# Performance work log

Measured on AMD Instinct MI355X. Metric: run time of the kernel, lower is better.

The kernel has to match this reference:

```python
import jax, jax.numpy as jnp
import numpy as np

B, N_NODES, D, H, L, DFF, K = 16, 512, 256, 8, 4, 1024, 128
DH = D // H


def setup_inputs() -> dict:
    key = jax.random.key(0)
    ks = jax.random.split(key, 16)
    x = jax.random.normal(ks[0], (B, N_NODES, D), jnp.float32)
    d = jax.random.uniform(ks[1], (B, N_NODES, N_NODES), jnp.float32)
    dist = 0.5 * (d + jnp.swapaxes(d, -1, -2))
    dist = dist * (1.0 - jnp.eye(N_NODES, dtype=jnp.float32))  # zero diagonal
    mask = jnp.ones((B, 1, N_NODES), dtype=bool)
    s = 0.02
    Wq = jax.random.normal(ks[2], (L, D, D), jnp.float32) * s
    Wk = jax.random.normal(ks[3], (L, D, D), jnp.float32) * s
    Wv = jax.random.normal(ks[4], (L, D, D), jnp.float32) * s
    Wo = jax.random.normal(ks[5], (L, D, D), jnp.float32) * s
    W1 = jax.random.normal(ks[6], (L, D, DFF), jnp.float32) * s
    W2 = jax.random.normal(ks[7], (L, DFF, D), jnp.float32) * s
    ln1_g = jnp.ones((L, D), jnp.float32)
    ln1_b = jnp.zeros((L, D), jnp.float32)
    ln2_g = jnp.ones((L, D), jnp.float32)
    ln2_b = jnp.zeros((L, D), jnp.float32)
    gamma = jnp.ones((D,), jnp.float32)
    beta = jnp.zeros((D,), jnp.float32)
    return dict(x=x, dist=dist, mask=mask, Wq=Wq, Wk=Wk, Wv=Wv, Wo=Wo, W1=W1, W2=W2,
                ln1_g=ln1_g, ln1_b=ln1_b, ln2_g=ln2_g, ln2_b=ln2_b, gamma=gamma, beta=beta)


def _ln(x, g, b, eps=1e-6):
    mu = jnp.mean(x, axis=-1, keepdims=True)
    var = jnp.mean((x - mu) ** 2, axis=-1, keepdims=True)
    return (x - mu) * jax.lax.rsqrt(var + eps) * g + b


def _afps(scores, dist, k):
    # scores: [H, n, n] attention probs; dist: [n, n]; mask assumed all-True.
    s = jnp.sum(jnp.mean(scores, axis=0), axis=-2)            # [n] column sums
    d = dist / jnp.max(dist) + (s / jnp.max(s))[:, None] * 0.1  # [n, n]
    n = d.shape[0]
    mind0 = d[:, 0]                                            # min dist to {0}
    sel0 = jnp.zeros((n,), bool).at[0].set(True)

    def body(carry, _):
        mind, sel = carry
        cand = jnp.where(sel, -jnp.inf, mind)  # exclude already-selected
        new = jnp.argmax(cand)
        return (jnp.minimum(mind, d[:, new]), sel.at[new].set(True)), new

    _, picks = jax.lax.scan(body, (mind0, sel0), None, length=k - 1)
    return jnp.concatenate([jnp.zeros((1,), picks.dtype), picks])  # [k]


def reference(x, dist, mask, Wq, Wk, Wv, Wo, W1, W2, ln1_g, ln1_b, ln2_g, ln2_b, gamma, beta):
    key_mask = mask[:, :, None, :]  # [B,1,1,n] broadcast over heads/queries
    inv_sqrt = np.float32(1.0 / np.sqrt(DH))
    scores = None
    for i in range(L):
        h = _ln(x, ln1_g[i], ln1_b[i])
        q = (h @ Wq[i]).reshape(B, N_NODES, H, DH).transpose(0, 2, 1, 3)
        kk = (h @ Wk[i]).reshape(B, N_NODES, H, DH).transpose(0, 2, 1, 3)
        v = (h @ Wv[i]).reshape(B, N_NODES, H, DH).transpose(0, 2, 1, 3)
        logits = jnp.einsum('bhqd,bhkd->bhqk', q, kk) * inv_sqrt - dist[:, None]
        logits = jnp.where(key_mask, logits, jnp.float32(-1e9))
        scores = jax.nn.softmax(logits, axis=-1)               # [B,H,n,n]
        attn = jnp.einsum('bhqk,bhkd->bhqd', scores, v)
        x = x + attn.transpose(0, 2, 1, 3).reshape(B, N_NODES, D) @ Wo[i]
        h2 = _ln(x, ln2_g[i], ln2_b[i])
        x = x + jax.nn.gelu(h2 @ W1[i]) @ W2[i]
    # AFPS index selection runs under no_grad in the original
    idx = jax.vmap(lambda sc, dd: _afps(sc, dd, K))(
        jax.lax.stop_gradient(scores), jax.lax.stop_gradient(dist))  # [B,K]
    pooled = jnp.mean(jnp.take_along_axis(x, idx[:, :, None], axis=1), axis=1)  # [B,D]
    return _ln(pooled, gamma, beta)
```

## Files before the change

kernel.cpp:

```cpp
#include <hip/hip_runtime.h>
#include <hip/hip_bf16.h>
#include <math.h>

#define BB 16
#define NN 512
#define DD 256
#define HH 8
#define LL 4
#define DFF 1024
#define KSEL 128
#define DH 32

typedef __attribute__((ext_vector_type(8))) short bf16x8v;
typedef __attribute__((ext_vector_type(4))) float f32x4v;

static const size_t X_B    = 0;
static const size_t QKVB_B = 8388608;
static const size_t VT_B   = 20971520;
static const size_t FFN_B  = 8388608;
static const size_t H_B    = 25165824;
static const size_t ATT_B  = 29360128;
static const size_t WQKV_B = 33554432;
static const size_t WO_B   = 35127296;
static const size_t W1T_B  = 35651584;
static const size_t W2T_B  = 37748736;
static const size_t S_B    = 39845888;
static const size_t MAXD_B = 39878656;
static const size_t IDX_B  = 39878720;

__device__ __forceinline__ float gelu_f(float x) {
  float x3 = x * x * x;
  return 0.5f * x * (1.f + tanhf(0.7978845608028654f * (x + 0.044715f * x3)));
}

__device__ __forceinline__ short bf16raw(float v) {
  __hip_bfloat16 h = __float2bfloat16(v);
  return *reinterpret_cast<short*>(&h);
}

__device__ __forceinline__ float blk_sum_256(float v, float* stmp) {
  #pragma unroll
  for (int o = 32; o > 0; o >>= 1) v += __shfl_down(v, o, 64);
  if ((threadIdx.x & 63) == 0) stmp[threadIdx.x >> 6] = v;
  __syncthreads();
  if (threadIdx.x == 0) stmp[0] = stmp[0] + stmp[1] + stmp[2] + stmp[3];
  __syncthreads();
  float r = stmp[0];
  __syncthreads();
  return r;
}

__global__ void copy_kernel(const float4* __restrict__ src, float4* __restrict__ dst, int n) {
  int i = blockIdx.x * blockDim.x + threadIdx.x;
  if (i < n) dst[i] = src[i];
}

__global__ __launch_bounds__(256) void cast_weights_kernel(
    const float* __restrict__ Wq, const float* __restrict__ Wk,
    const float* __restrict__ Wv, const float* __restrict__ Wo,
    const float* __restrict__ W1, const float* __restrict__ W2,
    __hip_bfloat16* __restrict__ qkvT, __hip_bfloat16* __restrict__ WoT,
    __hip_bfloat16* __restrict__ W1T, __hip_bfloat16* __restrict__ W2T) {
  int i = blockIdx.x * 256 + threadIdx.x;
  if (i < 786432) {
    int l = i / 196608, r = i % 196608;
    int n = r >> 8, k = r & 255;
    const float* src = (n < 256) ? Wq : (n < 512 ? Wk : Wv);
    qkvT[i] = __float2bfloat16(src[l * 65536 + k * 256 + (n & 255)]);
  } else if (i < 1048576) {
    int j = i - 786432;
    int l = j >> 16, r = j & 65535;
    int n = r >> 8, k = r & 255;
    WoT[j] = __float2bfloat16(Wo[l * 65536 + k * 256 + n]);
  } else if (i < 2097152) {
    int j = i - 1048576;
    int l = j >> 18, r = j & 262143;
    int n = r >> 8, k = r & 255;
    W1T[j] = __float2bfloat16(W1[l * 262144 + k * 1024 + n]);
  } else {
    int j = i - 2097152;
    int l = j >> 18, r = j & 262143;
    int n = r >> 10, k = r & 1023;
    W2T[j] = __float2bfloat16(W2[l * 262144 + k * 256 + n]);
  }
}

__global__ __launch_bounds__(256) void ln_cast_kernel(const float* __restrict__ in,
                                                      const float* __restrict__ g,
                                                      const float* __restrict__ bb,
                                                      __hip_bfloat16* __restrict__ out) {
  __shared__ float stmp[4];
  size_t row = blockIdx.x;
  int d = threadIdx.x;
  float v = in[row * DD + d];
  float mu = blk_sum_256(v, stmp) * (1.0f / DD);
  float diff = v - mu;
  float var = blk_sum_256(diff * diff, stmp) * (1.0f / DD);
  out[row * DD + d] = __float2bfloat16(diff * rsqrtf(var + 1e-6f) * g[d] + bb[d]);
}

template <int MODE>
__global__ __launch_bounds__(256) void mfma_gemm(const __hip_bfloat16* __restrict__ A,
                                                 const __hip_bfloat16* __restrict__ Bt,
                                                 const float* __restrict__ Res,
                                                 void* __restrict__ Cv,
                                                 __hip_bfloat16* __restrict__ Vto,
                                                 int M, int N, int Kd) {
  __shared__ short As[64 * 40];
  __shared__ short Bs[64 * 40];
  const int tid = threadIdx.x;
  const int w = tid >> 6, lane = tid & 63;
  const int m16 = lane & 15, quad = lane >> 4;
  const int bm = blockIdx.y << 6, bn = blockIdx.x << 6;
  const int srow = tid >> 2, scol = (tid & 3) << 3;

  f32x4v zero = {0.f, 0.f, 0.f, 0.f};
  f32x4v acc[4];
  #pragma unroll
  for (int nt = 0; nt < 4; ++nt) acc[nt] = zero;

  const short* Ag = (const short*)A;
  const short* Bg = (const short*)Bt;

  for (int k0 = 0; k0 < Kd; k0 += 32) {
    *(bf16x8v*)&As[srow * 40 + scol] =
        *(const bf16x8v*)(Ag + (size_t)(bm + srow) * Kd + k0 + scol);
    *(bf16x8v*)&Bs[srow * 40 + scol] =
        *(const bf16x8v*)(Bg + (size_t)(bn + srow) * Kd + k0 + scol);
    __syncthreads();
    bf16x8v af = *(bf16x8v*)&As[(w * 16 + m16) * 40 + (quad << 3)];
    #pragma unroll
    for (int nt = 0; nt < 4; ++nt) {
      bf16x8v bf = *(bf16x8v*)&Bs[(nt * 16 + m16) * 40 + (quad << 3)];
      acc[nt] = __builtin_amdgcn_mfma_f32_16x16x32_bf16(af, bf, acc[nt], 0, 0, 0);
    }
    __syncthreads();
  }

  const int erow = bm + w * 16 + quad * 4;
  #pragma unroll
  for (int nt = 0; nt < 4; ++nt) {
    int col = bn + nt * 16 + m16;
    if (MODE == 3) {
      if (col < 512) {
        #pragma unroll
        for (int r = 0; r < 4; ++r)
          ((__hip_bfloat16*)Cv)[(size_t)(erow + r) * 768 + col] =
              __float2bfloat16(acc[nt][r]);
      } else {
        short4 pk;
        pk.x = bf16raw(acc[nt][0]); pk.y = bf16raw(acc[nt][1]);
        pk.z = bf16raw(acc[nt][2]); pk.w = bf16raw(acc[nt][3]);
        int bb2 = erow >> 9, key = erow & 511, dim = col - 512;
        *(short4*)((short*)Vto + (size_t)bb2 * 131072 + (size_t)dim * 512 + key) = pk;
      }
    } else {
      #pragma unroll
      for (int r = 0; r < 4; ++r) {
        float v = acc[nt][r];
        size_t off = (size_t)(erow + r) * N + col;
        if (MODE == 1) ((float*)Cv)[off] = v + Res[off];
        else ((__hip_bfloat16*)Cv)[off] = __float2bfloat16(gelu_f(v));
      }
    }
  }
}

__global__ __launch_bounds__(512) void attn_kernel(const __hip_bfloat16* __restrict__ qkvb,
                                                   const __hip_bfloat16* __restrict__ vt,
                                                   const float* __restrict__ dist,
                                                   __hip_bfloat16* __restrict__ outg,
                                                   float* __restrict__ s_acc,
                                                   int accum) {
  __shared__ float Pf[8][16 * 36];
  const int tid = threadIdx.x;
  const int h = tid >> 6, lane = tid & 63;
  const int m16 = lane & 15, quad = lane >> 4;
  const int b = blockIdx.y;
  const int qbase = blockIdx.x * 16;
  const float scale = 0.17677669529663687f;
  const f32x4v zero = {0.f, 0.f, 0.f, 0.f};

  const short* qkvs = (const short*)qkvb;
  const short* vts = (const short*)vt + (size_t)b * 131072;
  float* Pw = Pf[h];

  bf16x8v qf = *(const bf16x8v*)(qkvs + ((size_t)(b * NN + qbase + m16)) * 768 + h * 32 + (quad << 3));

  int drow[4];
  #pragma unroll
  for (int r = 0; r < 4; ++r) drow[r] = (b * NN + qbase + quad * 4 + r) * NN;

  f32x4v accO0 = zero, accO1 = zero;
  float laccL[4] = {0.f, 0.f, 0.f, 0.f};

  for (int t0 = 0; t0 < NN; t0 += 32) {
    bf16x8v kf0 = *(const bf16x8v*)(qkvs + ((size_t)(b * NN + t0 + m16)) * 768 + 256 + h * 32 + (quad << 3));
    bf16x8v kf1 = *(const bf16x8v*)(qkvs + ((size_t)(b * NN + t0 + 16 + m16)) * 768 + 256 + h * 32 + (quad << 3));
    f32x4v s0 = __builtin_amdgcn_mfma_f32_16x16x32_bf16(qf, kf0, zero, 0, 0, 0);
    f32x4v s1 = __builtin_amdgcn_mfma_f32_16x16x32_bf16(qf, kf1, zero, 0, 0, 0);
    #pragma unroll
    for (int r = 0; r < 4; ++r) {
      float e0 = __expf(fmaf(s0[r], scale, -dist[drow[r] + t0 + m16]));
      float e1 = __expf(fmaf(s1[r], scale, -dist[drow[r] + t0 + 16 + m16]));
      laccL[r] += e0 + e1;
      Pw[(quad * 4 + r) * 36 + m16] = e0;
      Pw[(quad * 4 + r) * 36 + 16 + m16] = e1;
    }
    bf16x8v pfr;
    {
      const float* pr = &Pw[m16 * 36 + (quad << 3)];
      float4 pa = *(const float4*)pr;
      float4 pb = *(const float4*)(pr + 4);
      pfr[0] = bf16raw(pa.x); pfr[1] = bf16raw(pa.y);
      pfr[2] = bf16raw(pa.z); pfr[3] = bf16raw(pa.w);
      pfr[4] = bf16raw(pb.x); pfr[5] = bf16raw(pb.y);
      pfr[6] = bf16raw(pb.z); pfr[7] = bf16raw(pb.w);
    }
    bf16x8v vf0 = *(const bf16x8v*)(vts + (size_t)(h * 32 + m16) * 512 + t0 + (quad << 3));
    bf16x8v vf1 = *(const bf16x8v*)(vts + (size_t)(h * 32 + 16 + m16) * 512 + t0 + (quad << 3));
    accO0 = __builtin_amdgcn_mfma_f32_16x16x32_bf16(pfr, vf0, accO0, 0, 0, 0);
    accO1 = __builtin_amdgcn_mfma_f32_16x16x32_bf16(pfr, vf1, accO1, 0, 0, 0);
  }

  float invl[4];
  #pragma unroll
  for (int r = 0; r < 4; ++r) {
    float t = laccL[r];
    t += __shfl_xor(t, 1, 64); t += __shfl_xor(t, 2, 64);
    t += __shfl_xor(t, 4, 64); t += __shfl_xor(t, 8, 64);
    invl[r] = 1.f / t;
  }

  #pragma unroll
  for (int r = 0; r < 4; ++r) {
    size_t orow = (size_t)(b * NN + qbase + quad * 4 + r) * DD + h * 32;
    outg[orow + m16] = __float2bfloat16(accO0[r] * invl[r]);
    outg[orow + 16 + m16] = __float2bfloat16(accO1[r] * invl[r]);
  }

  if (accum) {
    for (int t0 = 0; t0 < NN; t0 += 32) {
      bf16x8v kf0 = *(const bf16x8v*)(qkvs + ((size_t)(b * NN + t0 + m16)) * 768 + 256 + h * 32 + (quad << 3));
      bf16x8v kf1 = *(const bf16x8v*)(qkvs + ((size_t)(b * NN + t0 + 16 + m16)) * 768 + 256 + h * 32 + (quad << 3));
      f32x4v s0 = __builtin_amdgcn_mfma_f32_16x16x32_bf16(qf, kf0, zero, 0, 0, 0);
      f32x4v s1 = __builtin_amdgcn_mfma_f32_16x16x32_bf16(qf, kf1, zero, 0, 0, 0);
      float p0 = 0.f, p1 = 0.f;
      #pragma unroll
      for (int r = 0; r < 4; ++r) {
        p0 += __expf(fmaf(s0[r], scale, -dist[drow[r] + t0 + m16])) * invl[r];
        p1 += __expf(fmaf(s1[r], scale, -dist[drow[r] + t0 + 16 + m16])) * invl[r];
      }
      p0 += __shfl_xor(p0, 16, 64); p0 += __shfl_xor(p0, 32, 64);
      p1 += __shfl_xor(p1, 16, 64); p1 += __shfl_xor(p1, 32, 64);
      if (quad == 0) {
        atomicAdd(&s_acc[b * NN + t0 + m16], p0 * 0.125f);
        atomicAdd(&s_acc[b * NN + t0 + 16 + m16], p1 * 0.125f);
      }
    }
  }
}

__global__ __launch_bounds__(256) void maxd_kernel(const float* __restrict__ dist,
                                                   unsigned int* __restrict__ maxd) {
  const int b = blockIdx.y;
  const int tid = threadIdx.x;
  const float4* p = (const float4*)(dist + (size_t)b * NN * NN) +
                    blockIdx.x * 8192 + tid;
  float m = 0.f;
  #pragma unroll 8
  for (int i = 0; i < 32; ++i) {
    float4 v = p[i * 256];
    m = fmaxf(m, fmaxf(fmaxf(v.x, v.y), fmaxf(v.z, v.w)));
  }
  #pragma unroll
  for (int o = 32; o > 0; o >>= 1) m = fmaxf(m, __shfl_xor(m, o, 64));
  __shared__ float wm[4];
  if ((tid & 63) == 0) wm[tid >> 6] = m;
  __syncthreads();
  if (tid == 0) {
    float mm = fmaxf(fmaxf(wm[0], wm[1]), fmaxf(wm[2], wm[3]));
    atomicMax(&maxd[b], __float_as_uint(mm));
  }
}

__global__ __launch_bounds__(64) void afps_select_kernel(const float* __restrict__ dist,
                                                         const float* __restrict__ s,
                                                         const unsigned int* __restrict__ maxd,
                                                         int* __restrict__ idx_out) {
  const int b = blockIdx.x;
  const int lane = threadIdx.x;
  const float* db = dist + (size_t)b * NN * NN;

  float sv[8];
  float ms = 0.f;
  #pragma unroll
  for (int r = 0; r < 8; ++r) {
    sv[r] = s[b * NN + r * 64 + lane];
    ms = fmaxf(ms, sv[r]);
  }
  #pragma unroll
  for (int o = 32; o > 0; o >>= 1) ms = fmaxf(ms, __shfl_xor(ms, o, 64));

  const float invmaxd = 1.0f / __uint_as_float(maxd[b]);
  float sn[8], mind[8];
  #pragma unroll
  for (int r = 0; r < 8; ++r) {
    sn[r] = (sv[r] / ms) * 0.1f;
    mind[r] = db[r * 64 + lane] * invmaxd + sn[r];
  }
  unsigned selm = (lane == 0) ? 1u : 0u;
  if (lane == 0) idx_out[b * KSEL + 0] = 0;

  int specIdx = -1;
  float sreg[8];

  for (int it = 1; it < KSEL; ++it) {
    unsigned long long b1 = 0ull, b2 = 0ull;
    #pragma unroll
    for (int r = 0; r < 8; ++r) {
      unsigned long long pk =
          ((selm >> r) & 1u) ? 0ull
            : (((unsigned long long)__float_as_uint(mind[r])) << 32) |
              (unsigned)(511 - (r * 64 + lane));
      if (pk > b1) { b2 = b1; b1 = pk; }
      else if (pk > b2) b2 = pk;
    }
    #pragma unroll
    for (int o = 32; o > 0; o >>= 1) {
      unsigned long long o1 = __shfl_xor(b1, o, 64);
      unsigned long long o2 = __shfl_xor(b2, o, 64);
      unsigned long long n1 = b1 > o1 ? b1 : o1;
      unsigned long long lo = b1 > o1 ? o1 : b1;
      unsigned long long n2 = b2 > o2 ? b2 : o2;
      b2 = lo > n2 ? lo : n2;
      b1 = n1;
    }
    const int nw = 511 - (int)(unsigned)(b1 & 0xffffffffu);
    const int sec = 511 - (int)(unsigned)(b2 & 0xffffffffu);

    float rowv[8];
    if (nw == specIdx) {
      #pragma unroll
      for (int r = 0; r < 8; ++r) rowv[r] = sreg[r];
    } else {
      const float* row = db + (size_t)nw * NN;
      #pragma unroll
      for (int r = 0; r < 8; ++r) rowv[r] = row[r * 64 + lane];
    }
    {
      const float* srow = db + (size_t)sec * NN;
      #pragma unroll
      for (int r = 0; r < 8; ++r) sreg[r] = srow[r * 64 + lane];
      specIdx = sec;
    }
    if (lane == (nw & 63)) selm |= 1u << (nw >> 6);
    if (lane == 0) idx_out[b * KSEL + it] = nw;
    #pragma unroll
    for (int r = 0; r < 8; ++r)
      mind[r] = fminf(mind[r], fmaf(rowv[r], invmaxd, sn[r]));
  }
}

__global__ __launch_bounds__(256) void pool_ln_kernel(const float* __restrict__ x,
                                                      const int* __restrict__ idx,
                                                      const float* __restrict__ gamma,
                                                      const float* __restrict__ beta,
                                                      float* __restrict__ out) {
  __shared__ float stmp[4];
  __shared__ int sIdx[KSEL];
  const int b = blockIdx.x;
  const int d = threadIdx.x;
  if (d < KSEL) sIdx[d] = idx[b * KSEL + d];
  __syncthreads();
  float acc = 0.f;
  #pragma unroll 4
  for (int kk = 0; kk < KSEL; ++kk)
    acc += x[((size_t)b * NN + sIdx[kk]) * DD + d];
  float p = acc * (1.0f / KSEL);
  float mu = blk_sum_256(p, stmp) * (1.0f / DD);
  float diff = p - mu;
  float var = blk_sum_256(diff * diff, stmp) * (1.0f / DD);
  out[b * DD + d] = diff * rsqrtf(var + 1e-6f) * gamma[d] + beta[d];
}

extern "C" void kernel_launch(void* const* d_in, const int* in_sizes, int n_in,
                              void* d_out, int out_size, void* d_ws, size_t ws_size,
                              hipStream_t stream) {
  (void)in_sizes; (void)n_in; (void)out_size; (void)ws_size;
  const float* x_in  = (const float*)d_in[0];
  const float* dist  = (const float*)d_in[1];
  const float* Wq    = (const float*)d_in[3];
  const float* Wk    = (const float*)d_in[4];
  const float* Wv    = (const float*)d_in[5];
  const float* Wo    = (const float*)d_in[6];
  const float* W1    = (const float*)d_in[7];
  const float* W2    = (const float*)d_in[8];
  const float* ln1_g = (const float*)d_in[9];
  const float* ln1_b = (const float*)d_in[10];
  const float* ln2_g = (const float*)d_in[11];
  const float* ln2_b = (const float*)d_in[12];
  const float* gamma = (const float*)d_in[13];
  const float* beta  = (const float*)d_in[14];

  char* wsb = (char*)d_ws;
  float* x              = (float*)(wsb + X_B);
  __hip_bfloat16* qkvb  = (__hip_bfloat16*)(wsb + QKVB_B);
  __hip_bfloat16* vtb   = (__hip_bfloat16*)(wsb + VT_B);
  __hip_bfloat16* ffn   = (__hip_bfloat16*)(wsb + FFN_B);
  __hip_bfloat16* hb    = (__hip_bfloat16*)(wsb + H_B);
  __hip_bfloat16* ab    = (__hip_bfloat16*)(wsb + ATT_B);
  __hip_bfloat16* WqkvT = (__hip_bfloat16*)(wsb + WQKV_B);
  __hip_bfloat16* WoT   = (__hip_bfloat16*)(wsb + WO_B);
  __hip_bfloat16* W1T   = (__hip_bfloat16*)(wsb + W1T_B);
  __hip_bfloat16* W2T   = (__hip_bfloat16*)(wsb + W2T_B);
  float* sbuf = (float*)(wsb + S_B);
  unsigned int* maxdb = (unsigned int*)(wsb + MAXD_B);
  int*   idxb = (int*)(wsb + IDX_B);
  float* out  = (float*)d_out;

  copy_kernel<<<2048, 256, 0, stream>>>((const float4*)x_in, (float4*)x, 524288);
  hipMemsetAsync(sbuf, 0, BB * NN * sizeof(float) + 64, stream);
  cast_weights_kernel<<<12288, 256, 0, stream>>>(Wq, Wk, Wv, Wo, W1, W2,
                                                 WqkvT, WoT, W1T, W2T);
  maxd_kernel<<<dim3(8, BB), 256, 0, stream>>>(dist, maxdb);

  const int M = BB * NN;
  dim3 gqkv(768 / 64, M / 64);
  dim3 go(DD / 64, M / 64);
  dim3 gf(DFF / 64, M / 64);
  dim3 ga(NN / 16, BB);

  for (int l = 0; l < LL; ++l) {
    ln_cast_kernel<<<M, 256, 0, stream>>>(x, ln1_g + l * DD, ln1_b + l * DD, hb);
    mfma_gemm<3><<<gqkv, 256, 0, stream>>>(hb, WqkvT + (size_t)l * 768 * 256, nullptr,
                                           qkvb, vtb, M, 768, 256);
    attn_kernel<<<ga, 512, 0, stream>>>(qkvb, vtb, dist, ab, sbuf, (l == LL - 1) ? 1 : 0);
    if (l == LL - 1) {
      afps_select_kernel<<<BB, 64, 0, stream>>>(dist, sbuf, maxdb, idxb);
    }
    mfma_gemm<1><<<go, 256, 0, stream>>>(ab, WoT + (size_t)l * 65536, x, x, nullptr, M, DD, 256);
    ln_cast_kernel<<<M, 256, 0, stream>>>(x, ln2_g + l * DD, ln2_b + l * DD, hb);
    mfma_gemm<2><<<gf, 256, 0, stream>>>(hb, W1T + (size_t)l * 262144, nullptr,
                                         ffn, nullptr, M, DFF, 256);
    mfma_gemm<1><<<go, 256, 0, stream>>>(ffn, W2T + (size_t)l * 262144, x, x, nullptr, M, DD, 1024);
  }
  pool_ln_kernel<<<BB, 256, 0, stream>>>(x, idxb, gamma, beta, out);
}
```

Baseline: 700.5 us.

## Fuse LayerNorm into QKV/FFN1 GEMMs, drop input copy, deepen AFPS speculation

LayerNorm is now computed inside the GEMM prologue: each block normalizes its 64 rows of fp32 x into a full-K bf16 LDS tile, which removes the separate ln_cast kernel and the bf16 h buffer round trip. The initial copy of x_in into the workspace is removed by reading x_in directly in layer 0 and using it as the residual source. The AFPS selection loop now keeps two speculatively prefetched distance rows instead of one. The cost is that LN work is repeated across every N-tile block (12 or 16 times per row) and the A tile in LDS grows to about 33KB, which may reduce occupancy.

```diff
diff --git a/kernel.cpp b/kernel.cpp
--- a/kernel.cpp
+++ b/kernel.cpp
@@ -18,7 +18,6 @@
 static const size_t QKVB_B = 8388608;
 static const size_t VT_B   = 20971520;
 static const size_t FFN_B  = 8388608;
-static const size_t H_B    = 25165824;
 static const size_t ATT_B  = 29360128;
 static const size_t WQKV_B = 33554432;
 static const size_t WO_B   = 35127296;
@@ -50,10 +49,6 @@
   return r;
 }
 
-__global__ void copy_kernel(const float4* __restrict__ src, float4* __restrict__ dst, int n) {
-  int i = blockIdx.x * blockDim.x + threadIdx.x;
-  if (i < n) dst[i] = src[i];
-}
 
 __global__ __launch_bounds__(256) void cast_weights_kernel(
     const float* __restrict__ Wq, const float* __restrict__ Wk,
@@ -85,50 +80,68 @@
   }
 }
 
-__global__ __launch_bounds__(256) void ln_cast_kernel(const float* __restrict__ in,
-                                                      const float* __restrict__ g,
-                                                      const float* __restrict__ bb,
-                                                      __hip_bfloat16* __restrict__ out) {
-  __shared__ float stmp[4];
-  size_t row = blockIdx.x;
-  int d = threadIdx.x;
-  float v = in[row * DD + d];
-  float mu = blk_sum_256(v, stmp) * (1.0f / DD);
-  float diff = v - mu;
-  float var = blk_sum_256(diff * diff, stmp) * (1.0f / DD);
-  out[row * DD + d] = __float2bfloat16(diff * rsqrtf(var + 1e-6f) * g[d] + bb[d]);
-}
-
 template <int MODE>
-__global__ __launch_bounds__(256) void mfma_gemm(const __hip_bfloat16* __restrict__ A,
-                                                 const __hip_bfloat16* __restrict__ Bt,
-                                                 const float* __restrict__ Res,
-                                                 void* __restrict__ Cv,
-                                                 __hip_bfloat16* __restrict__ Vto,
-                                                 int M, int N, int Kd) {
-  __shared__ short As[64 * 40];
+__global__ __launch_bounds__(256) void ln_gemm(const float* __restrict__ Xf,
+                                               const float* __restrict__ g,
+                                               const float* __restrict__ bb,
+                                               const __hip_bfloat16* __restrict__ Bt,
+                                               void* __restrict__ Cv,
+                                               __hip_bfloat16* __restrict__ Vto,
+                                               int N) {
+  __shared__ short As[64 * 264];
   __shared__ short Bs[64 * 40];
   const int tid = threadIdx.x;
   const int w = tid >> 6, lane = tid & 63;
   const int m16 = lane & 15, quad = lane >> 4;
   const int bm = blockIdx.y << 6, bn = blockIdx.x << 6;
+
+  {
+    const int row = tid >> 2, seg = (tid & 3) << 6;
+    const float* xr = Xf + (size_t)(bm + row) * 256 + seg;
+    float s1 = 0.f;
+    #pragma unroll
+    for (int i = 0; i < 16; ++i) {
+      float4 v = ((const float4*)xr)[i];
+      s1 += v.x + v.y + v.z + v.w;
+    }
+    s1 += __shfl_xor(s1, 1, 64); s1 += __shfl_xor(s1, 2, 64);
+    const float mu = s1 * (1.f / 256.f);
+    float s2 = 0.f;
+    #pragma unroll
+    for (int i = 0; i < 16; ++i) {
+      float4 v = ((const float4*)xr)[i];
+      float a0 = v.x - mu, a1 = v.y - mu, a2 = v.z - mu, a3 = v.w - mu;
+      s2 += a0 * a0 + a1 * a1 + a2 * a2 + a3 * a3;
+    }
+    s2 += __shfl_xor(s2, 1, 64); s2 += __shfl_xor(s2, 2, 64);
+    const float rsig = rsqrtf(s2 * (1.f / 256.f) + 1e-6f);
+    short* dst = &As[row * 264 + seg];
+    #pragma unroll
+    for (int i = 0; i < 16; ++i) {
+      float4 v = ((const float4*)xr)[i];
+      float4 gg = ((const float4*)(g + seg))[i];
+      float4 bv = ((const float4*)(bb + seg))[i];
+      short4 o;
+      o.x = bf16raw((v.x - mu) * rsig * gg.x + bv.x);
+      o.y = bf16raw((v.y - mu) * rsig * gg.y + bv.y);
+      o.z = bf16raw((v.z - mu) * rsig * gg.z + bv.z);
+      o.w = bf16raw((v.w - mu) * rsig * gg.w + bv.w);
+      *(short4*)(dst + i * 4) = o;
+    }
+  }
+  __syncthreads();
+
+  f32x4v acc[4];
+  #pragma unroll
+  for (int nt = 0; nt < 4; ++nt) acc[nt] = (f32x4v){0.f, 0.f, 0.f, 0.f};
+  const short* Bg = (const short*)Bt;
   const int srow = tid >> 2, scol = (tid & 3) << 3;
 
-  f32x4v zero = {0.f, 0.f, 0.f, 0.f};
-  f32x4v acc[4];
-  #pragma unroll
-  for (int nt = 0; nt < 4; ++nt) acc[nt] = zero;
-
-  const short* Ag = (const short*)A;
-  const short* Bg = (const short*)Bt;
-
-  for (int k0 = 0; k0 < Kd; k0 += 32) {
-    *(bf16x8v*)&As[srow * 40 + scol] =
-        *(const bf16x8v*)(Ag + (size_t)(bm + srow) * Kd + k0 + scol);
+  for (int k0 = 0; k0 < 256; k0 += 32) {
     *(bf16x8v*)&Bs[srow * 40 + scol] =
-        *(const bf16x8v*)(Bg + (size_t)(bn + srow) * Kd + k0 + scol);
+        *(const bf16x8v*)(Bg + (size_t)(bn + srow) * 256 + k0 + scol);
     __syncthreads();
-    bf16x8v af = *(bf16x8v*)&As[(w * 16 + m16) * 40 + (quad << 3)];
+    bf16x8v af = *(bf16x8v*)&As[(w * 16 + m16) * 264 + k0 + (quad << 3)];
     #pragma unroll
     for (int nt = 0; nt < 4; ++nt) {
       bf16x8v bf = *(bf16x8v*)&Bs[(nt * 16 + m16) * 40 + (quad << 3)];
@@ -156,12 +169,56 @@
       }
     } else {
       #pragma unroll
-      for (int r = 0; r < 4; ++r) {
-        float v = acc[nt][r];
-        size_t off = (size_t)(erow + r) * N + col;
-        if (MODE == 1) ((float*)Cv)[off] = v + Res[off];
-        else ((__hip_bfloat16*)Cv)[off] = __float2bfloat16(gelu_f(v));
-      }
+      for (int r = 0; r < 4; ++r)
+        ((__hip_bfloat16*)Cv)[(size_t)(erow + r) * N + col] =
+            __float2bfloat16(gelu_f(acc[nt][r]));
+    }
+  }
+}
+
+__global__ __launch_bounds__(256) void mfma_gemm_res(const __hip_bfloat16* __restrict__ A,
+                                                     const __hip_bfloat16* __restrict__ Bt,
+                                                     const float* __restrict__ Res,
+                                                     float* __restrict__ C,
+                                                     int M, int N, int Kd) {
+  __shared__ short As[64 * 40];
+  __shared__ short Bs[64 * 40];
+  const int tid = threadIdx.x;
+  const int w = tid >> 6, lane = tid & 63;
+  const int m16 = lane & 15, quad = lane >> 4;
+  const int bm = blockIdx.y << 6, bn = blockIdx.x << 6;
+  const int srow = tid >> 2, scol = (tid & 3) << 3;
+
+  f32x4v acc[4];
+  #pragma unroll
+  for (int nt = 0; nt < 4; ++nt) acc[nt] = (f32x4v){0.f, 0.f, 0.f, 0.f};
+
+  const short* Ag = (const short*)A;
+  const short* Bg = (const short*)Bt;
+
+  for (int k0 = 0; k0 < Kd; k0 += 32) {
+    *(bf16x8v*)&As[srow * 40 + scol] =
+        *(const bf16x8v*)(Ag + (size_t)(bm + srow) * Kd + k0 + scol);
+    *(bf16x8v*)&Bs[srow * 40 + scol] =
+        *(const bf16x8v*)(Bg + (size_t)(bn + srow) * Kd + k0 + scol);
+    __syncthreads();
+    bf16x8v af = *(bf16x8v*)&As[(w * 16 + m16) * 40 + (quad << 3)];
+    #pragma unroll
+    for (int nt = 0; nt < 4; ++nt) {
+      bf16x8v bf = *(bf16x8v*)&Bs[(nt * 16 + m16) * 40 + (quad << 3)];
+      acc[nt] = __builtin_amdgcn_mfma_f32_16x16x32_bf16(af, bf, acc[nt], 0, 0, 0);
+    }
+    __syncthreads();
+  }
+
+  const int erow = bm + w * 16 + quad * 4;
+  #pragma unroll
+  for (int nt = 0; nt < 4; ++nt) {
+    int col = bn + nt * 16 + m16;
+    #pragma unroll
+    for (int r = 0; r < 4; ++r) {
+      size_t off = (size_t)(erow + r) * N + col;
+      C[off] = acc[nt][r] + Res[off];
     }
   }
 }
@@ -312,8 +369,8 @@
   unsigned selm = (lane == 0) ? 1u : 0u;
   if (lane == 0) idx_out[b * KSEL + 0] = 0;
 
-  int specIdx = -1;
-  float sreg[8];
+  int spec0 = -1, spec1 = -1;
+  float sreg0[8], sreg1[8];
 
   for (int it = 1; it < KSEL; ++it) {
     unsigned long long b1 = 0ull, b2 = 0ull;
@@ -340,19 +397,25 @@
     const int sec = 511 - (int)(unsigned)(b2 & 0xffffffffu);
 
     float rowv[8];
-    if (nw == specIdx) {
-      #pragma unroll
-      for (int r = 0; r < 8; ++r) rowv[r] = sreg[r];
+    if (nw == spec0) {
+      #pragma unroll
+      for (int r = 0; r < 8; ++r) rowv[r] = sreg0[r];
+    } else if (nw == spec1) {
+      #pragma unroll
+      for (int r = 0; r < 8; ++r) rowv[r] = sreg1[r];
     } else {
       const float* row = db + (size_t)nw * NN;
       #pragma unroll
       for (int r = 0; r < 8; ++r) rowv[r] = row[r * 64 + lane];
     }
     {
+      #pragma unroll
+      for (int r = 0; r < 8; ++r) sreg1[r] = sreg0[r];
+      spec1 = spec0;
       const float* srow = db + (size_t)sec * NN;
       #pragma unroll
-      for (int r = 0; r < 8; ++r) sreg[r] = srow[r * 64 + lane];
-      specIdx = sec;
+      for (int r = 0; r < 8; ++r) sreg0[r] = srow[r * 64 + lane];
+      spec0 = sec;
     }
     if (lane == (nw & 63)) selm |= 1u << (nw >> 6);
     if (lane == 0) idx_out[b * KSEL + it] = nw;
@@ -408,7 +471,6 @@
   __hip_bfloat16* qkvb  = (__hip_bfloat16*)(wsb + QKVB_B);
   __hip_bfloat16* vtb   = (__hip_bfloat16*)(wsb + VT_B);
   __hip_bfloat16* ffn   = (__hip_bfloat16*)(wsb + FFN_B);
-  __hip_bfloat16* hb    = (__hip_bfloat16*)(wsb + H_B);
   __hip_bfloat16* ab    = (__hip_bfloat16*)(wsb + ATT_B);
   __hip_bfloat16* WqkvT = (__hip_bfloat16*)(wsb + WQKV_B);
   __hip_bfloat16* WoT   = (__hip_bfloat16*)(wsb + WO_B);
@@ -419,7 +481,6 @@
   int*   idxb = (int*)(wsb + IDX_B);
   float* out  = (float*)d_out;
 
-  copy_kernel<<<2048, 256, 0, stream>>>((const float4*)x_in, (float4*)x, 524288);
   hipMemsetAsync(sbuf, 0, BB * NN * sizeof(float) + 64, stream);
   cast_weights_kernel<<<12288, 256, 0, stream>>>(Wq, Wk, Wv, Wo, W1, W2,
                                                  WqkvT, WoT, W1T, W2T);
@@ -432,18 +493,17 @@
   dim3 ga(NN / 16, BB);
 
   for (int l = 0; l < LL; ++l) {
-    ln_cast_kernel<<<M, 256, 0, stream>>>(x, ln1_g + l * DD, ln1_b + l * DD, hb);
-    mfma_gemm<3><<<gqkv, 256, 0, stream>>>(hb, WqkvT + (size_t)l * 768 * 256, nullptr,
-                                           qkvb, vtb, M, 768, 256);
+    const float* xsrc = (l == 0) ? x_in : x;
+    ln_gemm<3><<<gqkv, 256, 0, stream>>>(xsrc, ln1_g + l * DD, ln1_b + l * DD,
+                                         WqkvT + (size_t)l * 768 * 256, qkvb, vtb, 768);
     attn_kernel<<<ga, 512, 0, stream>>>(qkvb, vtb, dist, ab, sbuf, (l == LL - 1) ? 1 : 0);
     if (l == LL - 1) {
       afps_select_kernel<<<BB, 64, 0, stream>>>(dist, sbuf, maxdb, idxb);
     }
-    mfma_gemm<1><<<go, 256, 0, stream>>>(ab, WoT + (size_t)l * 65536, x, x, nullptr, M, DD, 256);
-    ln_cast_kernel<<<M, 256, 0, stream>>>(x, ln2_g + l * DD, ln2_b + l * DD, hb);
-    mfma_gemm<2><<<gf, 256, 0, stream>>>(hb, W1T + (size_t)l * 262144, nullptr,
-                                         ffn, nullptr, M, DFF, 256);
-    mfma_gemm<1><<<go, 256, 0, stream>>>(ffn, W2T + (size_t)l * 262144, x, x, nullptr, M, DD, 1024);
+    mfma_gemm_res<<<go, 256, 0, stream>>>(ab, WoT + (size_t)l * 65536, xsrc, x, M, DD, 256);
+    ln_gemm<2><<<gf, 256, 0, stream>>>(x, ln2_g + l * DD, ln2_b + l * DD,
+                                       W1T + (size_t)l * 262144, ffn, nullptr, 1024);
+    mfma_gemm_res<<<go, 256, 0, stream>>>(ffn, W2T + (size_t)l * 262144, x, x, M, DD, 1024);
   }
   pool_ln_kernel<<<BB, 256, 0, stream>>>(x, idxb, gamma, beta, out);
 }
```

Result: slower. 999.1 us (+42.6%).

## Fold AFPS into Wo GEMM grid, drop input copy, vectorize layernorm

Applied to the files above, without the earlier changes.

Removes the initial copy of x by having layer 0 read the input directly as the LN source and residual. Rewrites the layernorm cast kernel so that one wave handles a row with float4 loads and shuffle reductions, four rows per block, with no shared-memory barriers. Runs the serial AFPS selection as an extra row of blocks inside the last layer's Wo GEMM launch, so the single-wave selection loop overlaps with the GEMM instead of occupying its own launch. The extra row adds four waves of long-running work to the GEMM grid, which may lengthen the tail of that launch.

```diff
diff --git a/kernel.cpp b/kernel.cpp
--- a/kernel.cpp
+++ b/kernel.cpp
@@ -50,10 +50,6 @@
   return r;
 }
 
-__global__ void copy_kernel(const float4* __restrict__ src, float4* __restrict__ dst, int n) {
-  int i = blockIdx.x * blockDim.x + threadIdx.x;
-  if (i < n) dst[i] = src[i];
-}
 
 __global__ __launch_bounds__(256) void cast_weights_kernel(
     const float* __restrict__ Wq, const float* __restrict__ Wk,
@@ -89,20 +85,32 @@
                                                       const float* __restrict__ g,
                                                       const float* __restrict__ bb,
                                                       __hip_bfloat16* __restrict__ out) {
-  __shared__ float stmp[4];
-  size_t row = blockIdx.x;
-  int d = threadIdx.x;
-  float v = in[row * DD + d];
-  float mu = blk_sum_256(v, stmp) * (1.0f / DD);
-  float diff = v - mu;
-  float var = blk_sum_256(diff * diff, stmp) * (1.0f / DD);
-  out[row * DD + d] = __float2bfloat16(diff * rsqrtf(var + 1e-6f) * g[d] + bb[d]);
+  const int tid = threadIdx.x;
+  const int lane = tid & 63;
+  const size_t row = (size_t)blockIdx.x * 4 + (tid >> 6);
+  const float4 v = *(const float4*)(in + row * DD + lane * 4);
+  float s1 = v.x + v.y + v.z + v.w;
+  #pragma unroll
+  for (int o = 32; o > 0; o >>= 1) s1 += __shfl_xor(s1, o, 64);
+  const float mu = s1 * (1.f / DD);
+  const float d0 = v.x - mu, d1 = v.y - mu, d2 = v.z - mu, d3 = v.w - mu;
+  float s2 = d0 * d0 + d1 * d1 + d2 * d2 + d3 * d3;
+  #pragma unroll
+  for (int o = 32; o > 0; o >>= 1) s2 += __shfl_xor(s2, o, 64);
+  const float rsig = rsqrtf(s2 * (1.f / DD) + 1e-6f);
+  const float4 gg = *(const float4*)(g + lane * 4);
+  const float4 bv = *(const float4*)(bb + lane * 4);
+  short4 o;
+  o.x = bf16raw(d0 * rsig * gg.x + bv.x);
+  o.y = bf16raw(d1 * rsig * gg.y + bv.y);
+  o.z = bf16raw(d2 * rsig * gg.z + bv.z);
+  o.w = bf16raw(d3 * rsig * gg.w + bv.w);
+  *(short4*)((short*)out + row * DD + lane * 4) = o;
 }
 
 template <int MODE>
 __global__ __launch_bounds__(256) void mfma_gemm(const __hip_bfloat16* __restrict__ A,
                                                  const __hip_bfloat16* __restrict__ Bt,
-                                                 const float* __restrict__ Res,
                                                  void* __restrict__ Cv,
                                                  __hip_bfloat16* __restrict__ Vto,
                                                  int M, int N, int Kd) {
@@ -114,10 +122,9 @@
   const int bm = blockIdx.y << 6, bn = blockIdx.x << 6;
   const int srow = tid >> 2, scol = (tid & 3) << 3;
 
-  f32x4v zero = {0.f, 0.f, 0.f, 0.f};
   f32x4v acc[4];
   #pragma unroll
-  for (int nt = 0; nt < 4; ++nt) acc[nt] = zero;
+  for (int nt = 0; nt < 4; ++nt) acc[nt] = (f32x4v){0.f, 0.f, 0.f, 0.f};
 
   const short* Ag = (const short*)A;
   const short* Bg = (const short*)Bt;
@@ -156,14 +163,162 @@
       }
     } else {
       #pragma unroll
-      for (int r = 0; r < 4; ++r) {
-        float v = acc[nt][r];
-        size_t off = (size_t)(erow + r) * N + col;
-        if (MODE == 1) ((float*)Cv)[off] = v + Res[off];
-        else ((__hip_bfloat16*)Cv)[off] = __float2bfloat16(gelu_f(v));
-      }
-    }
-  }
+      for (int r = 0; r < 4; ++r)
+        ((__hip_bfloat16*)Cv)[(size_t)(erow + r) * N + col] =
+            __float2bfloat16(gelu_f(acc[nt][r]));
+    }
+  }
+}
+
+__device__ __forceinline__ void gemm_res_body(const __hip_bfloat16* __restrict__ A,
+                                              const __hip_bfloat16* __restrict__ Bt,
+                                              const float* __restrict__ Res,
+                                              float* __restrict__ C,
+                                              int N, int Kd,
+                                              short* As, short* Bs) {
+  const int tid = threadIdx.x;
+  const int w = tid >> 6, lane = tid & 63;
+  const int m16 = lane & 15, quad = lane >> 4;
+  const int bm = blockIdx.y << 6, bn = blockIdx.x << 6;
+  const int srow = tid >> 2, scol = (tid & 3) << 3;
+
+  f32x4v acc[4];
+  #pragma unroll
+  for (int nt = 0; nt < 4; ++nt) acc[nt] = (f32x4v){0.f, 0.f, 0.f, 0.f};
+
+  const short* Ag = (const short*)A;
+  const short* Bg = (const short*)Bt;
+
+  for (int k0 = 0; k0 < Kd; k0 += 32) {
+    *(bf16x8v*)&As[srow * 40 + scol] =
+        *(const bf16x8v*)(Ag + (size_t)(bm + srow) * Kd + k0 + scol);
+    *(bf16x8v*)&Bs[srow * 40 + scol] =
+        *(const bf16x8v*)(Bg + (size_t)(bn + srow) * Kd + k0 + scol);
+    __syncthreads();
+    bf16x8v af = *(bf16x8v*)&As[(w * 16 + m16) * 40 + (quad << 3)];
+    #pragma unroll
+    for (int nt = 0; nt < 4; ++nt) {
+      bf16x8v bf = *(bf16x8v*)&Bs[(nt * 16 + m16) * 40 + (quad << 3)];
+      acc[nt] = __builtin_amdgcn_mfma_f32_16x16x32_bf16(af, bf, acc[nt], 0, 0, 0);
+    }
+    __syncthreads();
+  }
+
+  const int erow = bm + w * 16 + quad * 4;
+  #pragma unroll
+  for (int nt = 0; nt < 4; ++nt) {
+    int col = bn + nt * 16 + m16;
+    #pragma unroll
+    for (int r = 0; r < 4; ++r) {
+      size_t off = (size_t)(erow + r) * N + col;
+      C[off] = acc[nt][r] + Res[off];
+    }
+  }
+}
+
+__global__ __launch_bounds__(256) void mfma_gemm_res(const __hip_bfloat16* __restrict__ A,
+                                                     const __hip_bfloat16* __restrict__ Bt,
+                                                     const float* __restrict__ Res,
+                                                     float* __restrict__ C,
+                                                     int N, int Kd) {
+  __shared__ short As[64 * 40];
+  __shared__ short Bs[64 * 40];
+  gemm_res_body(A, Bt, Res, C, N, Kd, As, Bs);
+}
+
+__device__ void afps_wave(int b, int lane,
+                          const float* __restrict__ dist,
+                          const float* __restrict__ s,
+                          const unsigned int* __restrict__ maxd,
+                          int* __restrict__ idx_out) {
+  const float* db = dist + (size_t)b * NN * NN;
+
+  float sv[8];
+  float ms = 0.f;
+  #pragma unroll
+  for (int r = 0; r < 8; ++r) {
+    sv[r] = s[b * NN + r * 64 + lane];
+    ms = fmaxf(ms, sv[r]);
+  }
+  #pragma unroll
+  for (int o = 32; o > 0; o >>= 1) ms = fmaxf(ms, __shfl_xor(ms, o, 64));
+
+  const float invmaxd = 1.0f / __uint_as_float(maxd[b]);
+  float sn[8], mind[8];
+  #pragma unroll
+  for (int r = 0; r < 8; ++r) {
+    sn[r] = (sv[r] / ms) * 0.1f;
+    mind[r] = db[r * 64 + lane] * invmaxd + sn[r];
+  }
+  unsigned selm = (lane == 0) ? 1u : 0u;
+  if (lane == 0) idx_out[b * KSEL + 0] = 0;
+
+  int specIdx = -1;
+  float sreg[8];
+
+  for (int it = 1; it < KSEL; ++it) {
+    unsigned long long b1 = 0ull, b2 = 0ull;
+    #pragma unroll
+    for (int r = 0; r < 8; ++r) {
+      unsigned long long pk =
+          ((selm >> r) & 1u) ? 0ull
+            : (((unsigned long long)__float_as_uint(mind[r])) << 32) |
+              (unsigned)(511 - (r * 64 + lane));
+      if (pk > b1) { b2 = b1; b1 = pk; }
+      else if (pk > b2) b2 = pk;
+    }
+    #pragma unroll
+    for (int o = 32; o > 0; o >>= 1) {
+      unsigned long long o1 = __shfl_xor(b1, o, 64);
+      unsigned long long o2 = __shfl_xor(b2, o, 64);
+      unsigned long long n1 = b1 > o1 ? b1 : o1;
+      unsigned long long lo = b1 > o1 ? o1 : b1;
+      unsigned long long n2 = b2 > o2 ? b2 : o2;
+      b2 = lo > n2 ? lo : n2;
+      b1 = n1;
+    }
+    const int nw = 511 - (int)(unsigned)(b1 & 0xffffffffu);
+    const int sec = 511 - (int)(unsigned)(b2 & 0xffffffffu);
+
+    float rowv[8];
+    if (nw == specIdx) {
+      #pragma unroll
+      for (int r = 0; r < 8; ++r) rowv[r] = sreg[r];
+    } else {
+      const float* row = db + (size_t)nw * NN;
+      #pragma unroll
+      for (int r = 0; r < 8; ++r) rowv[r] = row[r * 64 + lane];
+    }
+    {
+      const float* srow = db + (size_t)sec * NN;
+      #pragma unroll
+      for (int r = 0; r < 8; ++r) sreg[r] = srow[r * 64 + lane];
+      specIdx = sec;
+    }
+    if (lane == (nw & 63)) selm |= 1u << (nw >> 6);
+    if (lane == 0) idx_out[b * KSEL + it] = nw;
+    #pragma unroll
+    for (int r = 0; r < 8; ++r)
+      mind[r] = fminf(mind[r], fmaf(rowv[r], invmaxd, sn[r]));
+  }
+}
+
+__global__ __launch_bounds__(256) void wo_gemm_afps(const __hip_bfloat16* __restrict__ A,
+                                                    const __hip_bfloat16* __restrict__ Bt,
+                                                    const float* __restrict__ Res,
+                                                    float* __restrict__ C,
+                                                    const float* __restrict__ dist,
+                                                    const float* __restrict__ s,
+                                                    const unsigned int* __restrict__ maxd,
+                                                    int* __restrict__ idx_out) {
+  __shared__ short As[64 * 40];
+  __shared__ short Bs[64 * 40];
+  if (blockIdx.y == 128) {
+    const int b = blockIdx.x * 4 + (threadIdx.x >> 6);
+    afps_wave(b, threadIdx.x & 63, dist, s, maxd, idx_out);
+    return;
+  }
+  gemm_res_body(A, Bt, Res, C, DD, 256, As, Bs);
 }
 
 __global__ __launch_bounds__(512) void attn_kernel(const __hip_bfloat16* __restrict__ qkvb,
@@ -281,84 +436,6 @@
   if (tid == 0) {
     float mm = fmaxf(fmaxf(wm[0], wm[1]), fmaxf(wm[2], wm[3]));
     atomicMax(&maxd[b], __float_as_uint(mm));
-  }
-}
-
-__global__ __launch_bounds__(64) void afps_select_kernel(const float* __restrict__ dist,
-                                                         const float* __restrict__ s,
-                                                         const unsigned int* __restrict__ maxd,
-                                                         int* __restrict__ idx_out) {
-  const int b = blockIdx.x;
-  const int lane = threadIdx.x;
-  const float* db = dist + (size_t)b * NN * NN;
-
-  float sv[8];
-  float ms = 0.f;
-  #pragma unroll
-  for (int r = 0; r < 8; ++r) {
-    sv[r] = s[b * NN + r * 64 + lane];
-    ms = fmaxf(ms, sv[r]);
-  }
-  #pragma unroll
-  for (int o = 32; o > 0; o >>= 1) ms = fmaxf(ms, __shfl_xor(ms, o, 64));
-
-  const float invmaxd = 1.0f / __uint_as_float(maxd[b]);
-  float sn[8], mind[8];
-  #pragma unroll
-  for (int r = 0; r < 8; ++r) {
-    sn[r] = (sv[r] / ms) * 0.1f;
-    mind[r] = db[r * 64 + lane] * invmaxd + sn[r];
-  }
-  unsigned selm = (lane == 0) ? 1u : 0u;
-  if (lane == 0) idx_out[b * KSEL + 0] = 0;
-
-  int specIdx = -1;
-  float sreg[8];
-
-  for (int it = 1; it < KSEL; ++it) {
-    unsigned long long b1 = 0ull, b2 = 0ull;
-    #pragma unroll
-    for (int r = 0; r < 8; ++r) {
-      unsigned long long pk =
-          ((selm >> r) & 1u) ? 0ull
-            : (((unsigned long long)__float_as_uint(mind[r])) << 32) |
-              (unsigned)(511 - (r * 64 + lane));
-      if (pk > b1) { b2 = b1; b1 = pk; }
-      else if (pk > b2) b2 = pk;
-    }
-    #pragma unroll
-    for (int o = 32; o > 0; o >>= 1) {
-      unsigned long long o1 = __shfl_xor(b1, o, 64);
-      unsigned long long o2 = __shfl_xor(b2, o, 64);
-      unsigned long long n1 = b1 > o1 ? b1 : o1;
-      unsigned long long lo = b1 > o1 ? o1 : b1;
-      unsigned long long n2 = b2 > o2 ? b2 : o2;
-      b2 = lo > n2 ? lo : n2;
-      b1 = n1;
-    }
-    const int nw = 511 - (int)(unsigned)(b1 & 0xffffffffu);
-    const int sec = 511 - (int)(unsigned)(b2 & 0xffffffffu);
-
-    float rowv[8];
-    if (nw == specIdx) {
-      #pragma unroll
-      for (int r = 0; r < 8; ++r) rowv[r] = sreg[r];
-    } else {
-      const float* row = db + (size_t)nw * NN;
-      #pragma unroll
-      for (int r = 0; r < 8; ++r) rowv[r] = row[r * 64 + lane];
-    }
-    {
-      const float* srow = db + (size_t)sec * NN;
-      #pragma unroll
-      for (int r = 0; r < 8; ++r) sreg[r] = srow[r * 64 + lane];
-      specIdx = sec;
-    }
-    if (lane == (nw & 63)) selm |= 1u << (nw >> 6);
-    if (lane == 0) idx_out[b * KSEL + it] = nw;
-    #pragma unroll
-    for (int r = 0; r < 8; ++r)
-      mind[r] = fminf(mind[r], fmaf(rowv[r], invmaxd, sn[r]));
   }
 }
 
@@ -419,7 +496,6 @@
   int*   idxb = (int*)(wsb + IDX_B);
   float* out  = (float*)d_out;
 
-  copy_kernel<<<2048, 256, 0, stream>>>((const float4*)x_in, (float4*)x, 524288);
   hipMemsetAsync(sbuf, 0, BB * NN * sizeof(float) + 64, stream);
   cast_weights_kernel<<<12288, 256, 0, stream>>>(Wq, Wk, Wv, Wo, W1, W2,
                                                  WqkvT, WoT, W1T, W2T);
@@ -428,22 +504,26 @@
   const int M = BB * NN;
   dim3 gqkv(768 / 64, M / 64);
   dim3 go(DD / 64, M / 64);
+  dim3 goA(DD / 64, M / 64 + 1);
   dim3 gf(DFF / 64, M / 64);
   dim3 ga(NN / 16, BB);
 
   for (int l = 0; l < LL; ++l) {
-    ln_cast_kernel<<<M, 256, 0, stream>>>(x, ln1_g + l * DD, ln1_b + l * DD, hb);
-    mfma_gemm<3><<<gqkv, 256, 0, stream>>>(hb, WqkvT + (size_t)l * 768 * 256, nullptr,
+    const float* xsrc = (l == 0) ? x_in : x;
+    ln_cast_kernel<<<M / 4, 256, 0, stream>>>(xsrc, ln1_g + l * DD, ln1_b + l * DD, hb);
+    mfma_gemm<3><<<gqkv, 256, 0, stream>>>(hb, WqkvT + (size_t)l * 768 * 256,
                                            qkvb, vtb, M, 768, 256);
     attn_kernel<<<ga, 512, 0, stream>>>(qkvb, vtb, dist, ab, sbuf, (l == LL - 1) ? 1 : 0);
     if (l == LL - 1) {
-      afps_select_kernel<<<BB, 64, 0, stream>>>(dist, sbuf, maxdb, idxb);
-    }
-    mfma_gemm<1><<<go, 256, 0, stream>>>(ab, WoT + (size_t)l * 65536, x, x, nullptr, M, DD, 256);
-    ln_cast_kernel<<<M, 256, 0, stream>>>(x, ln2_g + l * DD, ln2_b + l * DD, hb);
-    mfma_gemm<2><<<gf, 256, 0, stream>>>(hb, W1T + (size_t)l * 262144, nullptr,
+      wo_gemm_afps<<<goA, 256, 0, stream>>>(ab, WoT + (size_t)l * 65536, xsrc, x,
+                                            dist, sbuf, maxdb, idxb);
+    } else {
+      mfma_gemm_res<<<go, 256, 0, stream>>>(ab, WoT + (size_t)l * 65536, xsrc, x, DD, 256);
+    }
+    ln_cast_kernel<<<M / 4, 256, 0, stream>>>(x, ln2_g + l * DD, ln2_b + l * DD, hb);
+    mfma_gemm<2><<<gf, 256, 0, stream>>>(hb, W1T + (size_t)l * 262144,
                                          ffn, nullptr, M, DFF, 256);
-    mfma_gemm<1><<<go, 256, 0, stream>>>(ffn, W2T + (size_t)l * 262144, x, x, nullptr, M, DD, 1024);
+    mfma_gemm_res<<<go, 256, 0, stream>>>(ffn, W2T + (size_t)l * 262144, x, x, DD, 1024);
   }
   pool_ln_kernel<<<BB, 256, 0, stream>>>(x, idxb, gamma, beta, out);
 }
```

Result: no change. 686.9 us (-1.9%).
